# Kernel tuning notes

Measured on AMD Instinct MI355X. Metric: run time of the kernel, lower is better.

Reference implementation:

```python
import jax, jax.numpy as jnp
import numpy as np

N_NODES = 100000
HIDDEN = 128
N_EDGES = 1600000


def setup_inputs() -> dict:
    key = jax.random.key(0)
    k_x, k_w, k_r, k_c = jax.random.split(key, 4)
    x = jax.random.normal(k_x, (4, N_NODES, HIDDEN), dtype=jnp.float32)
    W = jax.random.normal(k_w, (HIDDEN, HIDDEN), dtype=jnp.float32) * 0.05
    b = jnp.zeros((HIDDEN,), dtype=jnp.float32)
    # COO edge list of the block-diagonal adjacency (scipy.sparse.block_diag in original)
    rows = jax.random.randint(k_r, (N_EDGES,), 0, N_NODES, dtype=jnp.int64)
    cols = jax.random.randint(k_c, (N_EDGES,), 0, N_NODES, dtype=jnp.int64)
    return {"x": x, "W": W, "b": b, "rows": rows, "cols": cols}


def reference(x, W, b, rows, cols):
    n_nodes = x.shape[1]
    beta = x[3, :, 0]   # [N]
    gamma = x[3, :, 1]  # [N]
    # linear + sigmoid on S/I/R channels: [3, N, H]
    sir = jax.nn.sigmoid(jnp.einsum('snh,oh->sno', x[:3], W) + b)
    S, I = sir[0], sir[1]
    # AI[r] += I[c] for each edge (r, c) of block-diagonal adjacency
    AI = jax.ops.segment_sum(I[cols], rows, num_segments=n_nodes)
    dS = -beta[:, None] * AI * S
    dI = -dS - gamma[:, None] * I
    dR = gamma[:, None] * I
    return jnp.stack((dS, dI, dR, jnp.zeros_like(dS)))
```

## Files before the change

kernel.cpp:

```cpp
#include <hip/hip_runtime.h>
#include <math.h>

#define HD 128
#define BM 128
#define ELLW 48

typedef short bf16x8 __attribute__((ext_vector_type(8)));
typedef float f32x4 __attribute__((ext_vector_type(4)));
typedef _Float16 h16x2 __attribute__((ext_vector_type(2)));
typedef unsigned short u16;

static __device__ __forceinline__ u16 f2bf(float f) {
  unsigned int u = __float_as_uint(f);
  u += 0x7FFF + ((u >> 16) & 1);
  return (u16)(u >> 16);
}
static __device__ __forceinline__ float bf2f(u16 s) {
  return __uint_as_float(((unsigned int)s) << 16);
}

__global__ void __launch_bounds__(256) zero_kernel(float4* __restrict__ p, long n4) {
  long i = (long)blockIdx.x * blockDim.x + threadIdx.x;
  long stride = (long)gridDim.x * blockDim.x;
  float4 z = make_float4(0.f, 0.f, 0.f, 0.f);
  for (; i < n4; i += stride) p[i] = z;
}

__global__ void __launch_bounds__(512, 4) fill_gemm(
    const float* __restrict__ x, const float* __restrict__ W,
    const float* __restrict__ b, float* __restrict__ S,
    _Float16* __restrict__ Ih, int n_nodes,
    const int* __restrict__ rows, const int* __restrict__ cols,
    int* __restrict__ cnt, int* __restrict__ ell,
    int n_edges, int fblocks) {
  __shared__ u16 Wh[HD * HD];
  __shared__ u16 Wl[HD * HD];

  int tid = threadIdx.x;
  int nrows = 2 * n_nodes;
  if (blockIdx.x < fblocks) {
    int i = blockIdx.x * 512 + tid;
    int stride = fblocks * 512;
    for (; i < n_edges; i += stride) {
      int r = rows[i];
      int c = cols[i];
      int p = atomicAdd(&cnt[r], 1);
      if (p < ELLW) ell[(long)r * ELLW + p] = c;
    }
    return;
  }

  for (int idx = tid; idx < HD * (HD / 8); idx += 512) {
    int r = idx >> 4;
    int c = idx & 15;
    const float4* src = (const float4*)(W + r * HD + c * 8);
    float4 a0 = src[0], a1 = src[1];
    float f[8] = {a0.x, a0.y, a0.z, a0.w, a1.x, a1.y, a1.z, a1.w};
    union { u16 s[8]; uint4 v; } Ph, Pl;
#pragma unroll
    for (int i = 0; i < 8; ++i) {
      u16 h = f2bf(f[i]);
      Ph.s[i] = h;
      Pl.s[i] = f2bf(f[i] - bf2f(h));
    }
    int dst = r * HD + ((c ^ (r & 15)) << 3);
    *(uint4*)&Wh[dst] = Ph.v;
    *(uint4*)&Wl[dst] = Pl.v;
  }
  __syncthreads();

  int w = tid >> 6;
  int l = tid & 63;
  int lr = l & 15;
  int lk = l >> 4;
  int rbase = (blockIdx.x - fblocks) * BM + w * 16;
  int arow = rbase + lr;
  bool rowok = arow < nrows;

  bf16x8 ah[4], al[4];
#pragma unroll
  for (int s = 0; s < 4; ++s) {
    float f[8] = {0.f, 0.f, 0.f, 0.f, 0.f, 0.f, 0.f, 0.f};
    if (rowok) {
      const float4* src = (const float4*)(x + (long)arow * HD + (s * 4 + lk) * 8);
      float4 a0 = src[0], a1 = src[1];
      f[0] = a0.x; f[1] = a0.y; f[2] = a0.z; f[3] = a0.w;
      f[4] = a1.x; f[5] = a1.y; f[6] = a1.z; f[7] = a1.w;
    }
    union { u16 s16[8]; bf16x8 v; } Ph, Pl;
#pragma unroll
    for (int i = 0; i < 8; ++i) {
      u16 h = f2bf(f[i]);
      Ph.s16[i] = h;
      Pl.s16[i] = f2bf(f[i] - bf2f(h));
    }
    ah[s] = Ph.v;
    al[s] = Pl.v;
  }

#pragma unroll
  for (int ct = 0; ct < 8; ++ct) {
    int col = ct * 16 + lr;
    f32x4 acc = {0.f, 0.f, 0.f, 0.f};
#pragma unroll
    for (int s = 0; s < 4; ++s) {
      int cb = ((s * 4 + lk) ^ lr) << 3;
      bf16x8 bh = *(const bf16x8*)&Wh[col * HD + cb];
      bf16x8 bl = *(const bf16x8*)&Wl[col * HD + cb];
      acc = __builtin_amdgcn_mfma_f32_16x16x32_bf16(ah[s], bh, acc, 0, 0, 0);
      acc = __builtin_amdgcn_mfma_f32_16x16x32_bf16(al[s], bh, acc, 0, 0, 0);
      acc = __builtin_amdgcn_mfma_f32_16x16x32_bf16(ah[s], bl, acc, 0, 0, 0);
    }
    float bb = b[col];
#pragma unroll
    for (int j = 0; j < 4; ++j) {
      int grow = rbase + lk * 4 + j;
      if (grow < nrows) {
        float v = acc[j] + bb;
        float sg = 1.f / (1.f + __expf(-v));
        if (grow < n_nodes)
          S[(long)grow * HD + col] = sg;
        else
          Ih[(long)(grow - n_nodes) * HD + col] = (_Float16)sg;
      }
    }
  }
}

__global__ void __launch_bounds__(256) gather_finalize(const float* __restrict__ S,
                                                       const _Float16* __restrict__ Ih,
                                                       const float* __restrict__ x3,
                                                       const int* __restrict__ cnt,
                                                       const int* __restrict__ ell,
                                                       float* __restrict__ out,
                                                       int n_nodes) {
  int node = blockIdx.x * 4 + (threadIdx.x >> 6);
  if (node >= n_nodes) return;
  int lane = threadIdx.x & 63;

  int deg = cnt[node];
  deg = min(deg, ELLW);
  int myc = (lane < deg) ? ell[(long)node * ELLW + lane] : 0;

  float2 acc = make_float2(0.f, 0.f);
  int j = 0;
  for (; j + 3 < deg; j += 4) {
    int c0 = __shfl(myc, j);
    int c1 = __shfl(myc, j + 1);
    int c2 = __shfl(myc, j + 2);
    int c3 = __shfl(myc, j + 3);
    h16x2 v0 = ((const h16x2*)(Ih + (long)c0 * HD))[lane];
    h16x2 v1 = ((const h16x2*)(Ih + (long)c1 * HD))[lane];
    h16x2 v2 = ((const h16x2*)(Ih + (long)c2 * HD))[lane];
    h16x2 v3 = ((const h16x2*)(Ih + (long)c3 * HD))[lane];
    acc.x += ((float)v0.x + (float)v1.x) + ((float)v2.x + (float)v3.x);
    acc.y += ((float)v0.y + (float)v1.y) + ((float)v2.y + (float)v3.y);
  }
  for (; j < deg; ++j) {
    int c0 = __shfl(myc, j);
    h16x2 v0 = ((const h16x2*)(Ih + (long)c0 * HD))[lane];
    acc.x += (float)v0.x;
    acc.y += (float)v0.y;
  }

  float beta  = x3[(long)node * HD + 0];
  float gamma = x3[(long)node * HD + 1];
  float2 s = ((const float2*)(S + (long)node * HD))[lane];
  h16x2 ih = ((const h16x2*)(Ih + (long)node * HD))[lane];
  float2 ii = make_float2((float)ih.x, (float)ih.y);

  float2 dS, dI, dR;
  dS.x = -beta * acc.x * s.x;
  dS.y = -beta * acc.y * s.y;
  dI.x = -dS.x - gamma * ii.x;
  dI.y = -dS.y - gamma * ii.y;
  dR.x = gamma * ii.x;
  dR.y = gamma * ii.y;

  long p = (long)node * (HD / 2) + lane;
  long plane = (long)n_nodes * (HD / 2);
  float2* o = (float2*)out;
  o[p] = dS;
  o[plane + p] = dI;
  o[2 * plane + p] = dR;
  o[3 * plane + p] = make_float2(0.f, 0.f);
}

extern "C" void kernel_launch(void* const* d_in, const int* in_sizes, int n_in,
                              void* d_out, int out_size, void* d_ws, size_t ws_size,
                              hipStream_t stream) {
  const float* x = (const float*)d_in[0];
  const float* W = (const float*)d_in[1];
  const float* b = (const float*)d_in[2];
  const int* rows = (const int*)d_in[3];
  const int* cols = (const int*)d_in[4];
  float* out = (float*)d_out;

  int n_nodes = in_sizes[0] / (4 * HD);
  int n_edges = in_sizes[3];
  int nrows = 2 * n_nodes;

  float* S = (float*)d_ws;
  _Float16* Ih = (_Float16*)(S + (long)n_nodes * HD);
  int* ib = (int*)(Ih + (long)n_nodes * HD);
  int npad = (n_nodes + 7) & ~3;
  int* cnt = ib;
  int* ell = cnt + npad;

  zero_kernel<<<128, 256, 0, stream>>>((float4*)cnt, npad / 4);

  int gblocks = (nrows + BM - 1) / BM;
  int fblocks = 192;
  fill_gemm<<<fblocks + gblocks, 512, 0, stream>>>(
      x, W, b, S, Ih, n_nodes, rows, cols, cnt, ell, n_edges, fblocks);

  int gfb = (n_nodes + 3) / 4;
  gather_finalize<<<gfb, 256, 0, stream>>>(S, Ih, x + 3 * (long)n_nodes * HD,
                                           cnt, ell, out, n_nodes);
}
```

Before: 504.0 us.

## Make GEMM blocks persistent with atomic tile counter and enlarge fill grid

```diff
diff --git a/kernel.cpp b/kernel.cpp
--- a/kernel.cpp
+++ b/kernel.cpp
@@ -31,17 +31,19 @@
     const float* __restrict__ b, float* __restrict__ S,
     _Float16* __restrict__ Ih, int n_nodes,
     const int* __restrict__ rows, const int* __restrict__ cols,
-    int* __restrict__ cnt, int* __restrict__ ell,
-    int n_edges, int fblocks) {
+    int* __restrict__ cnt, int* __restrict__ ell, int* __restrict__ tilectr,
+    int ntiles, int n_edges, int fblocks) {
   __shared__ u16 Wh[HD * HD];
   __shared__ u16 Wl[HD * HD];
 
   int tid = threadIdx.x;
   int nrows = 2 * n_nodes;
+
   if (blockIdx.x < fblocks) {
-    int i = blockIdx.x * 512 + tid;
+    int base = blockIdx.x * 512 + tid;
     int stride = fblocks * 512;
-    for (; i < n_edges; i += stride) {
+#pragma unroll 4
+    for (int i = base; i < n_edges; i += stride) {
       int r = rows[i];
       int c = cols[i];
       int p = atomicAdd(&cnt[r], 1);
@@ -69,59 +71,69 @@
   }
   __syncthreads();
 
+  __shared__ int stile;
   int w = tid >> 6;
   int l = tid & 63;
   int lr = l & 15;
   int lk = l >> 4;
-  int rbase = (blockIdx.x - fblocks) * BM + w * 16;
-  int arow = rbase + lr;
-  bool rowok = arow < nrows;
-
-  bf16x8 ah[4], al[4];
-#pragma unroll
-  for (int s = 0; s < 4; ++s) {
-    float f[8] = {0.f, 0.f, 0.f, 0.f, 0.f, 0.f, 0.f, 0.f};
-    if (rowok) {
-      const float4* src = (const float4*)(x + (long)arow * HD + (s * 4 + lk) * 8);
-      float4 a0 = src[0], a1 = src[1];
-      f[0] = a0.x; f[1] = a0.y; f[2] = a0.z; f[3] = a0.w;
-      f[4] = a1.x; f[5] = a1.y; f[6] = a1.z; f[7] = a1.w;
-    }
-    union { u16 s16[8]; bf16x8 v; } Ph, Pl;
-#pragma unroll
-    for (int i = 0; i < 8; ++i) {
-      u16 h = f2bf(f[i]);
-      Ph.s16[i] = h;
-      Pl.s16[i] = f2bf(f[i] - bf2f(h));
-    }
-    ah[s] = Ph.v;
-    al[s] = Pl.v;
-  }
-
-#pragma unroll
-  for (int ct = 0; ct < 8; ++ct) {
-    int col = ct * 16 + lr;
-    f32x4 acc = {0.f, 0.f, 0.f, 0.f};
+
+  for (;;) {
+    if (tid == 0) stile = atomicAdd(tilectr, 1);
+    __syncthreads();
+    int tile = stile;
+    __syncthreads();
+    if (tile >= ntiles) break;
+
+    int rbase = tile * BM + w * 16;
+    int arow = rbase + lr;
+    bool rowok = arow < nrows;
+
+    bf16x8 ah[4], al[4];
 #pragma unroll
     for (int s = 0; s < 4; ++s) {
-      int cb = ((s * 4 + lk) ^ lr) << 3;
-      bf16x8 bh = *(const bf16x8*)&Wh[col * HD + cb];
-      bf16x8 bl = *(const bf16x8*)&Wl[col * HD + cb];
-      acc = __builtin_amdgcn_mfma_f32_16x16x32_bf16(ah[s], bh, acc, 0, 0, 0);
-      acc = __builtin_amdgcn_mfma_f32_16x16x32_bf16(al[s], bh, acc, 0, 0, 0);
-      acc = __builtin_amdgcn_mfma_f32_16x16x32_bf16(ah[s], bl, acc, 0, 0, 0);
-    }
-    float bb = b[col];
-#pragma unroll
-    for (int j = 0; j < 4; ++j) {
-      int grow = rbase + lk * 4 + j;
-      if (grow < nrows) {
-        float v = acc[j] + bb;
-        float sg = 1.f / (1.f + __expf(-v));
-        if (grow < n_nodes)
-          S[(long)grow * HD + col] = sg;
-        else
-          Ih[(long)(grow - n_nodes) * HD + col] = (_Float16)sg;
+      float f[8] = {0.f, 0.f, 0.f, 0.f, 0.f, 0.f, 0.f, 0.f};
+      if (rowok) {
+        const float4* src = (const float4*)(x + (long)arow * HD + (s * 4 + lk) * 8);
+        float4 a0 = src[0], a1 = src[1];
+        f[0] = a0.x; f[1] = a0.y; f[2] = a0.z; f[3] = a0.w;
+        f[4] = a1.x; f[5] = a1.y; f[6] = a1.z; f[7] = a1.w;
+      }
+      union { u16 s16[8]; bf16x8 v; } Ph, Pl;
+#pragma unroll
+      for (int i = 0; i < 8; ++i) {
+        u16 h = f2bf(f[i]);
+        Ph.s16[i] = h;
+        Pl.s16[i] = f2bf(f[i] - bf2f(h));
+      }
+      ah[s] = Ph.v;
+      al[s] = Pl.v;
+    }
+
+#pragma unroll
+    for (int ct = 0; ct < 8; ++ct) {
+      int col = ct * 16 + lr;
+      f32x4 acc = {0.f, 0.f, 0.f, 0.f};
+#pragma unroll
+      for (int s = 0; s < 4; ++s) {
+        int cb = ((s * 4 + lk) ^ lr) << 3;
+        bf16x8 bh = *(const bf16x8*)&Wh[col * HD + cb];
+        bf16x8 bl = *(const bf16x8*)&Wl[col * HD + cb];
+        acc = __builtin_amdgcn_mfma_f32_16x16x32_bf16(ah[s], bh, acc, 0, 0, 0);
+        acc = __builtin_amdgcn_mfma_f32_16x16x32_bf16(al[s], bh, acc, 0, 0, 0);
+        acc = __builtin_amdgcn_mfma_f32_16x16x32_bf16(ah[s], bl, acc, 0, 0, 0);
+      }
+      float bb = b[col];
+#pragma unroll
+      for (int j = 0; j < 4; ++j) {
+        int grow = rbase + lk * 4 + j;
+        if (grow < nrows) {
+          float v = acc[j] + bb;
+          float sg = 1.f / (1.f + __expf(-v));
+          if (grow < n_nodes)
+            S[(long)grow * HD + col] = sg;
+          else
+            Ih[(long)(grow - n_nodes) * HD + col] = (_Float16)sg;
+        }
       }
     }
   }
@@ -199,20 +211,23 @@
   int n_nodes = in_sizes[0] / (4 * HD);
   int n_edges = in_sizes[3];
   int nrows = 2 * n_nodes;
+  int ntiles = (nrows + BM - 1) / BM;
 
   float* S = (float*)d_ws;
   _Float16* Ih = (_Float16*)(S + (long)n_nodes * HD);
   int* ib = (int*)(Ih + (long)n_nodes * HD);
   int npad = (n_nodes + 7) & ~3;
   int* cnt = ib;
-  int* ell = cnt + npad;
-
-  zero_kernel<<<128, 256, 0, stream>>>((float4*)cnt, npad / 4);
-
-  int gblocks = (nrows + BM - 1) / BM;
-  int fblocks = 192;
-  fill_gemm<<<fblocks + gblocks, 512, 0, stream>>>(
-      x, W, b, S, Ih, n_nodes, rows, cols, cnt, ell, n_edges, fblocks);
+  int* tilectr = cnt + npad;
+  int* ell = tilectr + 8;
+
+  zero_kernel<<<128, 256, 0, stream>>>((float4*)cnt, (npad + 8) / 4);
+
+  int fblocks = 320;
+  int gpb = 512;
+  fill_gemm<<<fblocks + gpb, 512, 0, stream>>>(
+      x, W, b, S, Ih, n_nodes, rows, cols, cnt, ell, tilectr,
+      ntiles, n_edges, fblocks);
 
   int gfb = (n_nodes + 3) / 4;
   gather_finalize<<<gfb, 256, 0, stream>>>(S, Ih, x + 3 * (long)n_nodes * HD,
```

After: 525.9 us. 4.4% more time.
